# Kernel optimization log

Measured on AMD Instinct MI355X. Metric: run time of the kernel, lower is better.

Reference implementation:

```python
import jax, jax.numpy as jnp
import numpy as np

N, E, D, H, C, G = 80000, 1280000, 64, 64, 5, 512


def setup_inputs() -> dict:
    key = jax.random.key(0)
    ks = jax.random.split(key, 8)
    h = jax.random.normal(ks[0], (N, D), jnp.float32)
    src = jax.random.randint(ks[1], (E,), 0, N)
    dst = jax.random.randint(ks[2], (E,), 0, N)
    graph_ids = jnp.sort(jax.random.randint(ks[3], (N,), 0, G))
    # Glorot-ish init for weights
    W1 = jax.random.normal(ks[4], (D, H), jnp.float32) * (1.0 / np.sqrt(D))
    b1 = jnp.zeros((H,), jnp.float32)
    W2 = jax.random.normal(ks[5], (H, H), jnp.float32) * (1.0 / np.sqrt(H))
    b2 = jnp.zeros((H,), jnp.float32)
    Wc = jax.random.normal(ks[6], (H, C), jnp.float32) * (1.0 / np.sqrt(H))
    bc = jnp.zeros((C,), jnp.float32)
    return dict(h=h, src=src, dst=dst, graph_ids=graph_ids,
                W1=W1, b1=b1, W2=W2, b2=b2, Wc=Wc, bc=bc, num_graphs=G)


def reference(h, src, dst, graph_ids, W1, b1, W2, b2, Wc, bc, num_graphs):
    n = h.shape[0]
    ones_e = jnp.ones(src.shape[0], h.dtype)
    # DGL GraphConv norm='both': symmetric normalization, degrees clamped to >=1
    out_deg = jnp.clip(jax.ops.segment_sum(ones_e, src, num_segments=n), 1.0)
    in_deg = jnp.clip(jax.ops.segment_sum(ones_e, dst, num_segments=n), 1.0)
    norm_src = jax.lax.rsqrt(out_deg)  # [N]
    norm_dst = jax.lax.rsqrt(in_deg)   # [N]

    def graph_conv(x, W, b):
        x = x * norm_src[:, None]                                   # scale by D_out^{-1/2}
        agg = jax.ops.segment_sum(x[src], dst, num_segments=n)      # sparse A^T x (copy_u + sum)
        agg = agg * norm_dst[:, None]                               # scale by D_in^{-1/2}
        return agg @ W + b

    h1 = jax.nn.relu(graph_conv(h, W1, b1))
    h2 = jax.nn.relu(graph_conv(h1, W2, b2))

    # dgl.mean_nodes: per-graph mean pooling over nodes
    cnt = jnp.clip(jax.ops.segment_sum(jnp.ones(n, h.dtype), graph_ids,
                                       num_segments=num_graphs), 1.0)
    hg = jax.ops.segment_sum(h2, graph_ids, num_segments=num_graphs) / cnt[:, None]
    return hg @ Wc + bc  # [G, C] logits
```

## Files before the change

### kernel.cpp

```cpp
#include <hip/hip_runtime.h>
#include <hip/hip_bf16.h>


#define NBK 160
#define HB  256
#define CAP 9216

typedef __attribute__((ext_vector_type(8))) short bf16x8;
typedef __attribute__((ext_vector_type(4))) float f32x4;

__device__ __forceinline__ float bflo(unsigned u) { return __uint_as_float(u << 16); }
__device__ __forceinline__ float bfhi(unsigned u) { return __uint_as_float(u & 0xffff0000u); }
__device__ __forceinline__ float bf1(unsigned short u) { return __uint_as_float((unsigned)u << 16); }
__device__ __forceinline__ unsigned short f2bf(float f) {
    unsigned u = __float_as_uint(f);
    return (unsigned short)((u + 0x7fff + ((u >> 16) & 1)) >> 16);
}
__device__ __forceinline__ unsigned packbf(float lo, float hi) {
    return (unsigned)f2bf(lo) | ((unsigned)f2bf(hi) << 16);
}

__global__ __launch_bounds__(256) void pA_scatter(
    const int* __restrict__ src, const int* __restrict__ dst,
    int* __restrict__ curD, int* __restrict__ curS,
    int* __restrict__ pack, unsigned short* __restrict__ sloc,
    const int* __restrict__ gids, int* __restrict__ goffs,
    int E, int NB, int N, int G)
{
    if (blockIdx.x >= HB) {
        int i = (blockIdx.x - HB) * 256 + threadIdx.x;
        if (i >= N) return;
        int b = gids[i];
        if (i == 0) {
            for (int g = 0; g <= b; g++) goffs[g] = 0;
        } else {
            int a = gids[i - 1];
            for (int g = a + 1; g <= b; g++) goffs[g] = i;
        }
        if (i == N - 1) {
            for (int g = b + 1; g <= G; g++) goffs[g] = N;
        }
        return;
    }
    __shared__ int hd[NBK], hs[NBK];
    int t = threadIdx.x;
    for (int i = t; i < NB; i += 256) { hd[i] = 0; hs[i] = 0; }
    __syncthreads();
    int chunk = (E + HB - 1) / HB;
    int s0 = blockIdx.x * chunk, s1 = min(E, s0 + chunk);
    int q0 = s0 >> 2, q1 = s1 >> 2;
    const int4* s4 = (const int4*)src;
    const int4* d4 = (const int4*)dst;
    for (int q = q0 + t; q < q1; q += 256) {
        int4 d = d4[q];
        int4 s = s4[q];
        atomicAdd(&hd[d.x >> 9], 1); atomicAdd(&hd[d.y >> 9], 1);
        atomicAdd(&hd[d.z >> 9], 1); atomicAdd(&hd[d.w >> 9], 1);
        atomicAdd(&hs[s.x >> 9], 1); atomicAdd(&hs[s.y >> 9], 1);
        atomicAdd(&hs[s.z >> 9], 1); atomicAdd(&hs[s.w >> 9], 1);
    }
    for (int i = (q1 << 2) + t; i < s1; i += 256) {
        atomicAdd(&hd[dst[i] >> 9], 1);
        atomicAdd(&hs[src[i] >> 9], 1);
    }
    __syncthreads();
    for (int b = t; b < NB; b += 256) {
        int cd = hd[b], cs = hs[b];
        hd[b] = cd ? atomicAdd(&curD[b], cd) : 0;
        hs[b] = cs ? atomicAdd(&curS[b], cs) : 0;
    }
    __syncthreads();
    for (int q = q0 + t; q < q1; q += 256) {
        int4 d = d4[q];
        int4 s = s4[q];
        #pragma unroll
        for (int j = 0; j < 4; j++) {
            int ss = j == 0 ? s.x : j == 1 ? s.y : j == 2 ? s.z : s.w;
            int dd = j == 0 ? d.x : j == 1 ? d.y : j == 2 ? d.z : d.w;
            int bd = dd >> 9, bs = ss >> 9;
            int pd = atomicAdd(&hd[bd], 1);
            int ps = atomicAdd(&hs[bs], 1);
            if (pd < CAP) pack[(size_t)bd * CAP + pd] = ((dd & 511) << 17) | ss;
            if (ps < CAP) sloc[(size_t)bs * CAP + ps] = (unsigned short)(ss & 511);
        }
    }
    for (int i = (q1 << 2) + t; i < s1; i += 256) {
        int s = src[i], d = dst[i];
        int bd = d >> 9, bs = s >> 9;
        int pd = atomicAdd(&hd[bd], 1);
        int ps = atomicAdd(&hs[bs], 1);
        if (pd < CAP) pack[(size_t)bd * CAP + pd] = ((d & 511) << 17) | s;
        if (ps < CAP) sloc[(size_t)bs * CAP + ps] = (unsigned short)(s & 511);
    }
}

__global__ __launch_bounds__(256) void p5_build(
    const int* __restrict__ pack, const unsigned short* __restrict__ sloc,
    const int* __restrict__ curD, const int* __restrict__ curS,
    int* __restrict__ col, int* __restrict__ row_offs, int* __restrict__ deg,
    float* __restrict__ nsrc, float* __restrict__ ndst,
    const float* __restrict__ h, unsigned short* __restrict__ xs,
    int N, int NB)
{
    __shared__ int hist[512];
    __shared__ float nsl[512];
    __shared__ int wt[4];
    int t = threadIdx.x;
    bool dmode = blockIdx.x < NB;
    int b = dmode ? blockIdx.x : blockIdx.x - NB;
    int n0 = b << 9, n1 = min(N, n0 + 512);
    hist[t] = 0; hist[t + 256] = 0;
    __syncthreads();
    int e0 = b * CAP;
    int tot = min(dmode ? curD[b] : curS[b], CAP);
    int e1 = e0 + tot;
    if (!dmode) {
        for (int i = e0 + t; i < e1; i += 256)
            atomicAdd(&hist[sloc[i]], 1);
        __syncthreads();
        for (int n = n0 + t; n < n1; n += 256) {
            float s = rsqrtf((float)max(hist[n - n0], 1));
            nsrc[n] = s;
            nsl[n - n0] = s;
        }
        __syncthreads();
        int cnt = n1 - n0;
        const float2* h2p = (const float2*)h;
        ushort2* xp = (ushort2*)xs;
        for (int i = t; i < cnt * 32; i += 256) {
            int node = i >> 5;
            float s = nsl[node];
            float2 v = h2p[(size_t)(n0 + node) * 32 + (i & 31)];
            ushort2 o;
            o.x = f2bf(v.x * s);
            o.y = f2bf(v.y * s);
            xp[(size_t)(n0 + node) * 32 + (i & 31)] = o;
        }
        return;
    }
    for (int i = e0 + t; i < e1; i += 256)
        atomicAdd(&hist[pack[i] >> 17], 1);
    __syncthreads();
    int c0 = hist[2 * t], c1 = hist[2 * t + 1];
    int v = c0 + c1;
    int lane = t & 63, w = t >> 6;
    int x = v;
    #pragma unroll
    for (int off = 1; off < 64; off <<= 1) {
        int y = __shfl_up(x, off);
        if (lane >= off) x += y;
    }
    if (lane == 63) wt[w] = x;
    __syncthreads();
    int bw = 0;
    for (int i = 0; i < w; i++) bw += wt[i];
    int excl = x - v + bw;
    int n = n0 + 2 * t;
    if (n < n1) {
        row_offs[n] = e0 + excl;
        deg[n] = c0;
        ndst[n] = rsqrtf((float)max(c0, 1));
    }
    if (n + 1 < n1) {
        row_offs[n + 1] = e0 + excl + c0;
        deg[n + 1] = c1;
        ndst[n + 1] = rsqrtf((float)max(c1, 1));
    }
    hist[2 * t] = excl;
    hist[2 * t + 1] = excl + c0;
    __syncthreads();
    for (int i = e0 + t; i < e1; i += 256) {
        int wd = pack[i];
        int pos = atomicAdd(&hist[wd >> 17], 1);
        col[e0 + pos] = wd & 0x1FFFF;
    }
}

__global__ __launch_bounds__(256) void agg_kernel(
    const unsigned short* __restrict__ z, unsigned short* __restrict__ y,
    const int* __restrict__ col, const int* __restrict__ row_offs,
    const int* __restrict__ deg, int N)
{
    int lane = threadIdx.x & 63;
    int sub  = lane >> 3;
    int li   = lane & 7;
    const uint4* x4 = (const uint4*)z;

    int wid = (blockIdx.x * 256 + threadIdx.x) >> 6;
    int nw  = (gridDim.x * 256) >> 6;

    int ro = 0, cnt = 0, idx = 0;
    if (wid < N) {
        ro = row_offs[wid];
        cnt = deg[wid];
        if (lane < min(cnt, 64)) idx = col[ro + lane];
    }
    for (int node = wid; node < N; node += nw) {
        int nnode = node + nw;
        int nro = 0, ncnt = 0;
        if (nnode < N) { nro = row_offs[nnode]; ncnt = deg[nnode]; }

        float a0=0.f,a1=0.f,a2=0.f,a3=0.f,a4=0.f,a5=0.f,a6=0.f,a7=0.f;
        int cc = 0;
        int cidx = idx;
        while (cc < cnt) {
            int m = min(cnt - cc, 64);
            for (int i = 0; i < m; i += 32) {
                int e1 = i + sub, e2 = i + 8 + sub, e3 = i + 16 + sub, e4 = i + 24 + sub;
                int s1 = __shfl(cidx, min(e1, m - 1));
                int s2 = __shfl(cidx, min(e2, m - 1));
                int s3 = __shfl(cidx, min(e3, m - 1));
                int s4 = __shfl(cidx, min(e4, m - 1));
                uint4 v1 = make_uint4(0u,0u,0u,0u), v2 = v1, v3 = v1, v4 = v1;
                if (e1 < m) v1 = x4[(size_t)s1 * 8 + li];
                if (e2 < m) v2 = x4[(size_t)s2 * 8 + li];
                if (e3 < m) v3 = x4[(size_t)s3 * 8 + li];
                if (e4 < m) v4 = x4[(size_t)s4 * 8 + li];
                a0 += bflo(v1.x); a1 += bfhi(v1.x);
                a2 += bflo(v1.y); a3 += bfhi(v1.y);
                a4 += bflo(v1.z); a5 += bfhi(v1.z);
                a6 += bflo(v1.w); a7 += bfhi(v1.w);
                a0 += bflo(v2.x); a1 += bfhi(v2.x);
                a2 += bflo(v2.y); a3 += bfhi(v2.y);
                a4 += bflo(v2.z); a5 += bfhi(v2.z);
                a6 += bflo(v2.w); a7 += bfhi(v2.w);
                a0 += bflo(v3.x); a1 += bfhi(v3.x);
                a2 += bflo(v3.y); a3 += bfhi(v3.y);
                a4 += bflo(v3.z); a5 += bfhi(v3.z);
                a6 += bflo(v3.w); a7 += bfhi(v3.w);
                a0 += bflo(v4.x); a1 += bfhi(v4.x);
                a2 += bflo(v4.y); a3 += bfhi(v4.y);
                a4 += bflo(v4.z); a5 += bfhi(v4.z);
                a6 += bflo(v4.w); a7 += bfhi(v4.w);
            }
            cc += 64;
            if (cc < cnt) cidx = (lane < min(cnt - cc, 64)) ? col[ro + cc + lane] : 0;
        }
        idx = 0;
        if (nnode < N && lane < min(ncnt, 64)) idx = col[nro + lane];

        #pragma unroll
        for (int off = 8; off <= 32; off <<= 1) {
            a0 += __shfl_xor(a0, off); a1 += __shfl_xor(a1, off);
            a2 += __shfl_xor(a2, off); a3 += __shfl_xor(a3, off);
            a4 += __shfl_xor(a4, off); a5 += __shfl_xor(a5, off);
            a6 += __shfl_xor(a6, off); a7 += __shfl_xor(a7, off);
        }
        if (sub == 0) {
            uint4 o;
            o.x = packbf(a0, a1);
            o.y = packbf(a2, a3);
            o.z = packbf(a4, a5);
            o.w = packbf(a6, a7);
            ((uint4*)y)[(size_t)node * 8 + li] = o;
        }
        ro = nro; cnt = ncnt;
    }
}

template<int POOL>
__global__ __launch_bounds__(256) void gemm_kernel(
    const unsigned short* __restrict__ A, const float* __restrict__ W,
    const float* __restrict__ b, const float* __restrict__ ndst,
    const float* __restrict__ nsrc, unsigned short* __restrict__ Z,
    const int* __restrict__ gids, float* __restrict__ gacc, int M)
{
    int t = threadIdx.x, lane = t & 63, w = t >> 6;
    int col = lane & 15, quad = lane >> 4;
    bf16x8 bfrag[4][2];
    #pragma unroll
    for (int nt = 0; nt < 4; nt++)
        #pragma unroll
        for (int ks = 0; ks < 2; ks++)
            #pragma unroll
            for (int j = 0; j < 8; j++)
                bfrag[nt][ks][j] =
                    (short)f2bf(W[(ks * 32 + quad * 8 + j) * 64 + nt * 16 + col]);
    float bias[4];
    #pragma unroll
    for (int nt = 0; nt < 4; nt++) bias[nt] = b[nt * 16 + col];

    int mbase = blockIdx.x * 64 + w * 16;
    if (mbase >= M) return;
    int row = min(mbase + col, M - 1);
    const uint4* a4 = (const uint4*)A;
    union { uint4 u; bf16x8 v; } a0, a1;
    a0.u = a4[(size_t)row * 8 + quad];
    a1.u = a4[(size_t)row * 8 + 4 + quad];

    float nd[4], ns[4];
    int gg[4];
    #pragma unroll
    for (int r = 0; r < 4; r++) {
        int m = min(mbase + quad * 4 + r, M - 1);
        nd[r] = ndst[m];
        ns[r] = POOL ? 1.f : nsrc[m];
        gg[r] = POOL ? gids[m] : 0;
    }
    bool uni = false;
    int g0 = 0;
    if (POOL) {
        g0 = gids[min(mbase, M - 1)];
        uni = (g0 == gids[min(mbase + 15, M - 1)]) && (mbase + 15 < M);
    }

    #pragma unroll
    for (int nt = 0; nt < 4; nt++) {
        f32x4 acc = {0.f, 0.f, 0.f, 0.f};
        acc = __builtin_amdgcn_mfma_f32_16x16x32_bf16(a0.v, bfrag[nt][0], acc, 0, 0, 0);
        acc = __builtin_amdgcn_mfma_f32_16x16x32_bf16(a1.v, bfrag[nt][1], acc, 0, 0, 0);
        if (POOL) {
            float vv[4];
            #pragma unroll
            for (int r = 0; r < 4; r++) {
                int m = mbase + quad * 4 + r;
                vv[r] = (m < M) ? fmaxf(nd[r] * acc[r] + bias[nt], 0.f) : 0.f;
            }
            if (uni) {
                float s = (vv[0] + vv[1]) + (vv[2] + vv[3]);
                s += __shfl_xor(s, 16);
                s += __shfl_xor(s, 32);
                if (quad == 0)
                    atomicAdd(&gacc[(size_t)g0 * 64 + nt * 16 + col], s);
            } else {
                #pragma unroll
                for (int r = 0; r < 4; r++) {
                    int m = mbase + quad * 4 + r;
                    if (m < M)
                        atomicAdd(&gacc[(size_t)gg[r] * 64 + nt * 16 + col], vv[r]);
                }
            }
        } else {
            #pragma unroll
            for (int r = 0; r < 4; r++) {
                int m = mbase + quad * 4 + r;
                if (m < M) {
                    float v = fmaxf(nd[r] * acc[r] + bias[nt], 0.f);
                    Z[(size_t)m * 64 + nt * 16 + col] = f2bf(v * ns[r]);
                }
            }
        }
    }
}

__global__ __launch_bounds__(64) void cls_kernel(
    const float* __restrict__ gacc, const int* __restrict__ goffs,
    const float* __restrict__ Wc, const float* __restrict__ bc,
    float* __restrict__ out, int G)
{
    int g = blockIdx.x;
    int lane = threadIdx.x;
    float cnt = (float)max(goffs[g + 1] - goffs[g], 1);
    float mean = gacc[(size_t)g * 64 + lane] / cnt;
    #pragma unroll
    for (int c = 0; c < 5; c++) {
        float p = mean * Wc[lane * 5 + c];
        #pragma unroll
        for (int off = 32; off; off >>= 1) p += __shfl_down(p, off);
        if (lane == 0) out[g * 5 + c] = p + bc[c];
    }
}

extern "C" void kernel_launch(void* const* d_in, const int* in_sizes, int n_in,
                              void* d_out, int out_size, void* d_ws, size_t ws_size,
                              hipStream_t stream)
{
    const float* h    = (const float*)d_in[0];
    const int*   src  = (const int*)d_in[1];
    const int*   dst  = (const int*)d_in[2];
    const int*   gids = (const int*)d_in[3];
    const float* W1   = (const float*)d_in[4];
    const float* b1   = (const float*)d_in[5];
    const float* W2   = (const float*)d_in[6];
    const float* b2   = (const float*)d_in[7];
    const float* Wc   = (const float*)d_in[8];
    const float* bc   = (const float*)d_in[9];
    float* out = (float*)d_out;

    const int N = in_sizes[0] / 64;
    const int E = in_sizes[1];
    const int G = out_size / 5;
    const int NB = (N + 511) >> 9;
    const int NBB = (N + 255) / 256;

    auto align = [](size_t x) { return (x + 255) & ~(size_t)255; };
    char* p = (char*)d_ws;
    int* curD    = (int*)p;
    int* curS    = curD + NBK;
    float* gacc  = (float*)(p + (size_t)2 * NBK * 4);
    size_t zbytes = (size_t)2 * NBK * 4 + (size_t)G * 64 * 4;
    p += align(zbytes);
    int* row_offs= (int*)p;            p += align((size_t)N * 4);
    int* deg     = (int*)p;            p += align((size_t)N * 4);
    float* nsrc  = (float*)p;          p += align((size_t)N * 4);
    float* ndst  = (float*)p;          p += align((size_t)N * 4);
    int* goffs   = (int*)p;            p += align((size_t)(G + 1) * 4);
    int* pack    = (int*)p;            p += align((size_t)NBK * CAP * 4);
    unsigned short* sloc = (unsigned short*)p; p += align((size_t)NBK * CAP * 2);
    int* cols    = (int*)p;            p += align((size_t)NBK * CAP * 4);
    unsigned short* xs  = (unsigned short*)p; p += align((size_t)N * 64 * 2);
    unsigned short* s1  = (unsigned short*)p; p += align((size_t)N * 64 * 2);
    unsigned short* h1s = (unsigned short*)p; p += align((size_t)N * 64 * 2);
    unsigned short* s2  = s1;

    hipMemsetAsync(curD, 0, zbytes, stream);

    pA_scatter<<<HB + NBB, 256, 0, stream>>>(src, dst, curD, curS, pack, sloc,
                                             gids, goffs, E, NB, N, G);
    p5_build<<<2 * NB, 256, 0, stream>>>(pack, sloc, curD, curS, cols,
                                         row_offs, deg, nsrc, ndst, h, xs, N, NB);

    agg_kernel<<<4096, 256, 0, stream>>>(xs, s1, cols, row_offs, deg, N);
    gemm_kernel<0><<<(N + 63) / 64, 256, 0, stream>>>(s1, W1, b1, ndst, nsrc,
                                                      h1s, nullptr, nullptr, N);
    agg_kernel<<<4096, 256, 0, stream>>>(h1s, s2, cols, row_offs, deg, N);
    gemm_kernel<1><<<(N + 63) / 64, 256, 0, stream>>>(s2, W2, b2, ndst, nullptr,
                                                      nullptr, gids, gacc, N);
    cls_kernel<<<G, 64, 0, stream>>>(gacc, goffs, Wc, bc, out, G);
}
```

Baseline: 216.5 us.

## Prefetch next node's first gathers in aggregation; fuse classifier into pooling GEMM

The aggregation kernel now issues the first 32 neighbor-row gathers for the next node before reducing and storing the current node. This hides some gather latency across loop iterations at the cost of extra live registers. Separately, the classifier kernel is removed. The last block of the pooling GEMM, chosen with a global ticket counter and threadfence, computes the per-graph means and logits, saving one launch but serializing that tail work onto a single block.

```diff
diff --git a/kernel.cpp b/kernel.cpp
--- a/kernel.cpp
+++ b/kernel.cpp
@@ -176,6 +176,12 @@
     }
 }
 
+#define UNPACK8S(v)                                       \
+    a0 += bflo(v.x); a1 += bfhi(v.x);                     \
+    a2 += bflo(v.y); a3 += bfhi(v.y);                     \
+    a4 += bflo(v.z); a5 += bfhi(v.z);                     \
+    a6 += bflo(v.w); a7 += bfhi(v.w);
+
 __global__ __launch_bounds__(256) void agg_kernel(
     const unsigned short* __restrict__ z, unsigned short* __restrict__ y,
     const int* __restrict__ col, const int* __restrict__ row_offs,
@@ -185,15 +191,27 @@
     int sub  = lane >> 3;
     int li   = lane & 7;
     const uint4* x4 = (const uint4*)z;
+    const uint4 z4 = make_uint4(0u, 0u, 0u, 0u);
 
     int wid = (blockIdx.x * 256 + threadIdx.x) >> 6;
     int nw  = (gridDim.x * 256) >> 6;
 
     int ro = 0, cnt = 0, idx = 0;
+    uint4 pv1 = z4, pv2 = z4, pv3 = z4, pv4 = z4;
     if (wid < N) {
         ro = row_offs[wid];
         cnt = deg[wid];
         if (lane < min(cnt, 64)) idx = col[ro + lane];
+        int m = min(cnt, 64), mm = min(m, 32);
+        int e1 = sub, e2 = 8 + sub, e3 = 16 + sub, e4 = 24 + sub;
+        int s1 = __shfl(idx, min(e1, m - 1) & 63);
+        int s2 = __shfl(idx, min(e2, m - 1) & 63);
+        int s3 = __shfl(idx, min(e3, m - 1) & 63);
+        int s4 = __shfl(idx, min(e4, m - 1) & 63);
+        if (e1 < mm) pv1 = x4[(size_t)s1 * 8 + li];
+        if (e2 < mm) pv2 = x4[(size_t)s2 * 8 + li];
+        if (e3 < mm) pv3 = x4[(size_t)s3 * 8 + li];
+        if (e4 < mm) pv4 = x4[(size_t)s4 * 8 + li];
     }
     for (int node = wid; node < N; node += nw) {
         int nnode = node + nw;
@@ -201,43 +219,58 @@
         if (nnode < N) { nro = row_offs[nnode]; ncnt = deg[nnode]; }
 
         float a0=0.f,a1=0.f,a2=0.f,a3=0.f,a4=0.f,a5=0.f,a6=0.f,a7=0.f;
-        int cc = 0;
-        int cidx = idx;
-        while (cc < cnt) {
-            int m = min(cnt - cc, 64);
-            for (int i = 0; i < m; i += 32) {
-                int e1 = i + sub, e2 = i + 8 + sub, e3 = i + 16 + sub, e4 = i + 24 + sub;
-                int s1 = __shfl(cidx, min(e1, m - 1));
-                int s2 = __shfl(cidx, min(e2, m - 1));
-                int s3 = __shfl(cidx, min(e3, m - 1));
-                int s4 = __shfl(cidx, min(e4, m - 1));
-                uint4 v1 = make_uint4(0u,0u,0u,0u), v2 = v1, v3 = v1, v4 = v1;
+        {
+            int m = min(cnt, 64);
+            UNPACK8S(pv1); UNPACK8S(pv2); UNPACK8S(pv3); UNPACK8S(pv4);
+            if (m > 32) {
+                int e1 = 32 + sub, e2 = 40 + sub, e3 = 48 + sub, e4 = 56 + sub;
+                int s1 = __shfl(idx, min(e1, m - 1));
+                int s2 = __shfl(idx, min(e2, m - 1));
+                int s3 = __shfl(idx, min(e3, m - 1));
+                int s4 = __shfl(idx, min(e4, m - 1));
+                uint4 v1 = z4, v2 = z4, v3 = z4, v4 = z4;
                 if (e1 < m) v1 = x4[(size_t)s1 * 8 + li];
                 if (e2 < m) v2 = x4[(size_t)s2 * 8 + li];
                 if (e3 < m) v3 = x4[(size_t)s3 * 8 + li];
                 if (e4 < m) v4 = x4[(size_t)s4 * 8 + li];
-                a0 += bflo(v1.x); a1 += bfhi(v1.x);
-                a2 += bflo(v1.y); a3 += bfhi(v1.y);
-                a4 += bflo(v1.z); a5 += bfhi(v1.z);
-                a6 += bflo(v1.w); a7 += bfhi(v1.w);
-                a0 += bflo(v2.x); a1 += bfhi(v2.x);
-                a2 += bflo(v2.y); a3 += bfhi(v2.y);
-                a4 += bflo(v2.z); a5 += bfhi(v2.z);
-                a6 += bflo(v2.w); a7 += bfhi(v2.w);
-                a0 += bflo(v3.x); a1 += bfhi(v3.x);
-                a2 += bflo(v3.y); a3 += bfhi(v3.y);
-                a4 += bflo(v3.z); a5 += bfhi(v3.z);
-                a6 += bflo(v3.w); a7 += bfhi(v3.w);
-                a0 += bflo(v4.x); a1 += bfhi(v4.x);
-                a2 += bflo(v4.y); a3 += bfhi(v4.y);
-                a4 += bflo(v4.z); a5 += bfhi(v4.z);
-                a6 += bflo(v4.w); a7 += bfhi(v4.w);
+                UNPACK8S(v1); UNPACK8S(v2); UNPACK8S(v3); UNPACK8S(v4);
             }
-            cc += 64;
-            if (cc < cnt) cidx = (lane < min(cnt - cc, 64)) ? col[ro + cc + lane] : 0;
-        }
+            int cc = 64;
+            while (cc < cnt) {
+                int m2 = min(cnt - cc, 64);
+                int cidx = (lane < m2) ? col[ro + cc + lane] : 0;
+                for (int i = 0; i < m2; i += 32) {
+                    int e1 = i + sub, e2 = i + 8 + sub, e3 = i + 16 + sub, e4 = i + 24 + sub;
+                    int s1 = __shfl(cidx, min(e1, m2 - 1));
+                    int s2 = __shfl(cidx, min(e2, m2 - 1));
+                    int s3 = __shfl(cidx, min(e3, m2 - 1));
+                    int s4 = __shfl(cidx, min(e4, m2 - 1));
+                    uint4 v1 = z4, v2 = z4, v3 = z4, v4 = z4;
+                    if (e1 < m2) v1 = x4[(size_t)s1 * 8 + li];
+                    if (e2 < m2) v2 = x4[(size_t)s2 * 8 + li];
+                    if (e3 < m2) v3 = x4[(size_t)s3 * 8 + li];
+                    if (e4 < m2) v4 = x4[(size_t)s4 * 8 + li];
+                    UNPACK8S(v1); UNPACK8S(v2); UNPACK8S(v3); UNPACK8S(v4);
+                }
+                cc += 64;
+            }
+        }
+
         idx = 0;
         if (nnode < N && lane < min(ncnt, 64)) idx = col[nro + lane];
+        pv1 = z4; pv2 = z4; pv3 = z4; pv4 = z4;
+        {
+            int m = min(ncnt, 64), mm = min(m, 32);
+            int e1 = sub, e2 = 8 + sub, e3 = 16 + sub, e4 = 24 + sub;
+            int s1 = __shfl(idx, min(e1, m - 1) & 63);
+            int s2 = __shfl(idx, min(e2, m - 1) & 63);
+            int s3 = __shfl(idx, min(e3, m - 1) & 63);
+            int s4 = __shfl(idx, min(e4, m - 1) & 63);
+            if (e1 < mm) pv1 = x4[(size_t)s1 * 8 + li];
+            if (e2 < mm) pv2 = x4[(size_t)s2 * 8 + li];
+            if (e3 < mm) pv3 = x4[(size_t)s3 * 8 + li];
+            if (e4 < mm) pv4 = x4[(size_t)s4 * 8 + li];
+        }
 
         #pragma unroll
         for (int off = 8; off <= 32; off <<= 1) {
@@ -263,8 +296,12 @@
     const unsigned short* __restrict__ A, const float* __restrict__ W,
     const float* __restrict__ b, const float* __restrict__ ndst,
     const float* __restrict__ nsrc, unsigned short* __restrict__ Z,
-    const int* __restrict__ gids, float* __restrict__ gacc, int M)
+    const int* __restrict__ gids, float* __restrict__ gacc,
+    int* __restrict__ ticket, const int* __restrict__ goffs,
+    const float* __restrict__ Wc, const float* __restrict__ bc,
+    float* __restrict__ out, int M, int G)
 {
+    __shared__ int lastf;
     int t = threadIdx.x, lane = t & 63, w = t >> 6;
     int col = lane & 15, quad = lane >> 4;
     bf16x8 bfrag[4][2];
@@ -281,83 +318,89 @@
     for (int nt = 0; nt < 4; nt++) bias[nt] = b[nt * 16 + col];
 
     int mbase = blockIdx.x * 64 + w * 16;
-    if (mbase >= M) return;
-    int row = min(mbase + col, M - 1);
-    const uint4* a4 = (const uint4*)A;
-    union { uint4 u; bf16x8 v; } a0, a1;
-    a0.u = a4[(size_t)row * 8 + quad];
-    a1.u = a4[(size_t)row * 8 + 4 + quad];
-
-    float nd[4], ns[4];
-    int gg[4];
-    #pragma unroll
-    for (int r = 0; r < 4; r++) {
-        int m = min(mbase + quad * 4 + r, M - 1);
-        nd[r] = ndst[m];
-        ns[r] = POOL ? 1.f : nsrc[m];
-        gg[r] = POOL ? gids[m] : 0;
-    }
-    bool uni = false;
-    int g0 = 0;
-    if (POOL) {
-        g0 = gids[min(mbase, M - 1)];
-        uni = (g0 == gids[min(mbase + 15, M - 1)]) && (mbase + 15 < M);
-    }
-
-    #pragma unroll
-    for (int nt = 0; nt < 4; nt++) {
-        f32x4 acc = {0.f, 0.f, 0.f, 0.f};
-        acc = __builtin_amdgcn_mfma_f32_16x16x32_bf16(a0.v, bfrag[nt][0], acc, 0, 0, 0);
-        acc = __builtin_amdgcn_mfma_f32_16x16x32_bf16(a1.v, bfrag[nt][1], acc, 0, 0, 0);
+    if (mbase < M) {
+        int row = min(mbase + col, M - 1);
+        const uint4* a4 = (const uint4*)A;
+        union { uint4 u; bf16x8 v; } a0, a1;
+        a0.u = a4[(size_t)row * 8 + quad];
+        a1.u = a4[(size_t)row * 8 + 4 + quad];
+
+        float nd[4], ns[4];
+        int gg[4];
+        #pragma unroll
+        for (int r = 0; r < 4; r++) {
+            int m = min(mbase + quad * 4 + r, M - 1);
+            nd[r] = ndst[m];
+            ns[r] = POOL ? 1.f : nsrc[m];
+            gg[r] = POOL ? gids[m] : 0;
+        }
+        bool uni = false;
+        int g0 = 0;
         if (POOL) {
-            float vv[4];
-            #pragma unroll
-            for (int r = 0; r < 4; r++) {
-                int m = mbase + quad * 4 + r;
-                vv[r] = (m < M) ? fmaxf(nd[r] * acc[r] + bias[nt], 0.f) : 0.f;
-            }
-            if (uni) {
-                float s = (vv[0] + vv[1]) + (vv[2] + vv[3]);
-                s += __shfl_xor(s, 16);
-                s += __shfl_xor(s, 32);
-                if (quad == 0)
-                    atomicAdd(&gacc[(size_t)g0 * 64 + nt * 16 + col], s);
+            g0 = gids[min(mbase, M - 1)];
+            uni = (g0 == gids[min(mbase + 15, M - 1)]) && (mbase + 15 < M);
+        }
+
+        #pragma unroll
+        for (int nt = 0; nt < 4; nt++) {
+            f32x4 acc = {0.f, 0.f, 0.f, 0.f};
+            acc = __builtin_amdgcn_mfma_f32_16x16x32_bf16(a0.v, bfrag[nt][0], acc, 0, 0, 0);
+            acc = __builtin_amdgcn_mfma_f32_16x16x32_bf16(a1.v, bfrag[nt][1], acc, 0, 0, 0);
+            if (POOL) {
+                float vv[4];
+                #pragma unroll
+                for (int r = 0; r < 4; r++) {
+                    int m = mbase + quad * 4 + r;
+                    vv[r] = (m < M) ? fmaxf(nd[r] * acc[r] + bias[nt], 0.f) : 0.f;
+                }
+                if (uni) {
+                    float s = (vv[0] + vv[1]) + (vv[2] + vv[3]);
+                    s += __shfl_xor(s, 16);
+                    s += __shfl_xor(s, 32);
+                    if (quad == 0)
+                        atomicAdd(&gacc[(size_t)g0 * 64 + nt * 16 + col], s);
+                } else {
+                    #pragma unroll
+                    for (int r = 0; r < 4; r++) {
+                        int m = mbase + quad * 4 + r;
+                        if (m < M)
+                            atomicAdd(&gacc[(size_t)gg[r] * 64 + nt * 16 + col], vv[r]);
+                    }
+                }
             } else {
                 #pragma unroll
                 for (int r = 0; r < 4; r++) {
                     int m = mbase + quad * 4 + r;
-                    if (m < M)
-                        atomicAdd(&gacc[(size_t)gg[r] * 64 + nt * 16 + col], vv[r]);
+                    if (m < M) {
+                        float v = fmaxf(nd[r] * acc[r] + bias[nt], 0.f);
+                        Z[(size_t)m * 64 + nt * 16 + col] = f2bf(v * ns[r]);
+                    }
                 }
             }
-        } else {
-            #pragma unroll
-            for (int r = 0; r < 4; r++) {
-                int m = mbase + quad * 4 + r;
-                if (m < M) {
-                    float v = fmaxf(nd[r] * acc[r] + bias[nt], 0.f);
-                    Z[(size_t)m * 64 + nt * 16 + col] = f2bf(v * ns[r]);
+        }
+    }
+
+    if (POOL) {
+        __threadfence();
+        __syncthreads();
+        if (t == 0) lastf = (atomicAdd(ticket, 1) == (int)gridDim.x - 1);
+        __syncthreads();
+        if (lastf) {
+            for (int g = w; g < G; g += 4) {
+                float cnt = (float)max(goffs[g + 1] - goffs[g], 1);
+                float v = __hip_atomic_load(&gacc[(size_t)g * 64 + lane],
+                                            __ATOMIC_RELAXED,
+                                            __HIP_MEMORY_SCOPE_AGENT);
+                float mean = v / cnt;
+                #pragma unroll
+                for (int c = 0; c < 5; c++) {
+                    float p = mean * Wc[lane * 5 + c];
+                    #pragma unroll
+                    for (int off = 32; off; off >>= 1) p += __shfl_down(p, off);
+                    if (lane == 0) out[g * 5 + c] = p + bc[c];
                 }
             }
         }
-    }
-}
-
-__global__ __launch_bounds__(64) void cls_kernel(
-    const float* __restrict__ gacc, const int* __restrict__ goffs,
-    const float* __restrict__ Wc, const float* __restrict__ bc,
-    float* __restrict__ out, int G)
-{
-    int g = blockIdx.x;
-    int lane = threadIdx.x;
-    float cnt = (float)max(goffs[g + 1] - goffs[g], 1);
-    float mean = gacc[(size_t)g * 64 + lane] / cnt;
-    #pragma unroll
-    for (int c = 0; c < 5; c++) {
-        float p = mean * Wc[lane * 5 + c];
-        #pragma unroll
-        for (int off = 32; off; off >>= 1) p += __shfl_down(p, off);
-        if (lane == 0) out[g * 5 + c] = p + bc[c];
     }
 }
 
@@ -387,8 +430,10 @@
     char* p = (char*)d_ws;
     int* curD    = (int*)p;
     int* curS    = curD + NBK;
-    float* gacc  = (float*)(p + (size_t)2 * NBK * 4);
-    size_t zbytes = (size_t)2 * NBK * 4 + (size_t)G * 64 * 4;
+    int* ticket  = curD + 2 * NBK;
+    size_t cur_bytes = align((size_t)(2 * NBK + 1) * 4);
+    float* gacc  = (float*)(p + cur_bytes);
+    size_t zbytes = cur_bytes + (size_t)G * 64 * 4;
     p += align(zbytes);
     int* row_offs= (int*)p;            p += align((size_t)N * 4);
     int* deg     = (int*)p;            p += align((size_t)N * 4);
@@ -411,10 +456,11 @@
                                          row_offs, deg, nsrc, ndst, h, xs, N, NB);
 
     agg_kernel<<<4096, 256, 0, stream>>>(xs, s1, cols, row_offs, deg, N);
-    gemm_kernel<0><<<(N + 63) / 64, 256, 0, stream>>>(s1, W1, b1, ndst, nsrc,
-                                                      h1s, nullptr, nullptr, N);
+    gemm_kernel<0><<<(N + 63) / 64, 256, 0, stream>>>(
+        s1, W1, b1, ndst, nsrc, h1s, nullptr, nullptr,
+        nullptr, nullptr, nullptr, nullptr, nullptr, N, G);
     agg_kernel<<<4096, 256, 0, stream>>>(h1s, s2, cols, row_offs, deg, N);
-    gemm_kernel<1><<<(N + 63) / 64, 256, 0, stream>>>(s2, W2, b2, ndst, nullptr,
-                                                      nullptr, gids, gacc, N);
-    cls_kernel<<<G, 64, 0, stream>>>(gacc, goffs, Wc, bc, out, G);
-}
+    gemm_kernel<1><<<(N + 63) / 64, 256, 0, stream>>>(
+        s2, W2, b2, ndst, nullptr, nullptr, gids, gacc,
+        ticket, goffs, Wc, bc, out, N, G);
+}
```

Measured after the change: 448.5 us. +107.1%, slower.

## Switch aggregation to lane-per-feature gathers with scalar readlane indices

Applied to the files above, without the earlier changes.

Restructures the gather-sum kernel so each of the 64 lanes owns one feature column and all lanes read the same neighbor row, broadcasting neighbor indices with readlane instead of shuffles. This removes the cross-lane shuffle-xor reduction and the uint4 repacking. In exchange each lane issues 2-byte loads, so there are many more load instructions per edge, although each row access is still one coalesced 128-byte read. Only 8 rows are in flight per iteration instead of 32.

```diff
diff --git a/kernel.cpp b/kernel.cpp
--- a/kernel.cpp
+++ b/kernel.cpp
@@ -15,9 +15,6 @@
 __device__ __forceinline__ unsigned short f2bf(float f) {
     unsigned u = __float_as_uint(f);
     return (unsigned short)((u + 0x7fff + ((u >> 16) & 1)) >> 16);
-}
-__device__ __forceinline__ unsigned packbf(float lo, float hi) {
-    return (unsigned)f2bf(lo) | ((unsigned)f2bf(hi) << 16);
 }
 
 __global__ __launch_bounds__(256) void pA_scatter(
@@ -182,78 +179,62 @@
     const int* __restrict__ deg, int N)
 {
     int lane = threadIdx.x & 63;
-    int sub  = lane >> 3;
-    int li   = lane & 7;
-    const uint4* x4 = (const uint4*)z;
 
     int wid = (blockIdx.x * 256 + threadIdx.x) >> 6;
     int nw  = (gridDim.x * 256) >> 6;
 
-    int ro = 0, cnt = 0, idx = 0;
+    int ro = 0, cnt = 0, cidx = 0;
     if (wid < N) {
         ro = row_offs[wid];
         cnt = deg[wid];
-        if (lane < min(cnt, 64)) idx = col[ro + lane];
+        if (lane < min(cnt, 64)) cidx = col[ro + lane];
     }
     for (int node = wid; node < N; node += nw) {
         int nnode = node + nw;
         int nro = 0, ncnt = 0;
         if (nnode < N) { nro = row_offs[nnode]; ncnt = deg[nnode]; }
 
-        float a0=0.f,a1=0.f,a2=0.f,a3=0.f,a4=0.f,a5=0.f,a6=0.f,a7=0.f;
+        float acc = 0.f;
         int cc = 0;
-        int cidx = idx;
+        int cur = cidx;
         while (cc < cnt) {
             int m = min(cnt - cc, 64);
-            for (int i = 0; i < m; i += 32) {
-                int e1 = i + sub, e2 = i + 8 + sub, e3 = i + 16 + sub, e4 = i + 24 + sub;
-                int s1 = __shfl(cidx, min(e1, m - 1));
-                int s2 = __shfl(cidx, min(e2, m - 1));
-                int s3 = __shfl(cidx, min(e3, m - 1));
-                int s4 = __shfl(cidx, min(e4, m - 1));
-                uint4 v1 = make_uint4(0u,0u,0u,0u), v2 = v1, v3 = v1, v4 = v1;
-                if (e1 < m) v1 = x4[(size_t)s1 * 8 + li];
-                if (e2 < m) v2 = x4[(size_t)s2 * 8 + li];
-                if (e3 < m) v3 = x4[(size_t)s3 * 8 + li];
-                if (e4 < m) v4 = x4[(size_t)s4 * 8 + li];
-                a0 += bflo(v1.x); a1 += bfhi(v1.x);
-                a2 += bflo(v1.y); a3 += bfhi(v1.y);
-                a4 += bflo(v1.z); a5 += bfhi(v1.z);
-                a6 += bflo(v1.w); a7 += bfhi(v1.w);
-                a0 += bflo(v2.x); a1 += bfhi(v2.x);
-                a2 += bflo(v2.y); a3 += bfhi(v2.y);
-                a4 += bflo(v2.z); a5 += bfhi(v2.z);
-                a6 += bflo(v2.w); a7 += bfhi(v2.w);
-                a0 += bflo(v3.x); a1 += bfhi(v3.x);
-                a2 += bflo(v3.y); a3 += bfhi(v3.y);
-                a4 += bflo(v3.z); a5 += bfhi(v3.z);
-                a6 += bflo(v3.w); a7 += bfhi(v3.w);
-                a0 += bflo(v4.x); a1 += bfhi(v4.x);
-                a2 += bflo(v4.y); a3 += bfhi(v4.y);
-                a4 += bflo(v4.z); a5 += bfhi(v4.z);
-                a6 += bflo(v4.w); a7 += bfhi(v4.w);
+            int e = 0;
+            for (; e + 8 <= m; e += 8) {
+                int s0 = __builtin_amdgcn_readlane(cur, e);
+                int s1 = __builtin_amdgcn_readlane(cur, e + 1);
+                int s2 = __builtin_amdgcn_readlane(cur, e + 2);
+                int s3 = __builtin_amdgcn_readlane(cur, e + 3);
+                int s4 = __builtin_amdgcn_readlane(cur, e + 4);
+                int s5 = __builtin_amdgcn_readlane(cur, e + 5);
+                int s6 = __builtin_amdgcn_readlane(cur, e + 6);
+                int s7 = __builtin_amdgcn_readlane(cur, e + 7);
+                unsigned short u0 = z[(size_t)s0 * 64 + lane];
+                unsigned short u1 = z[(size_t)s1 * 64 + lane];
+                unsigned short u2 = z[(size_t)s2 * 64 + lane];
+                unsigned short u3 = z[(size_t)s3 * 64 + lane];
+                unsigned short u4 = z[(size_t)s4 * 64 + lane];
+                unsigned short u5 = z[(size_t)s5 * 64 + lane];
+                unsigned short u6 = z[(size_t)s6 * 64 + lane];
+                unsigned short u7 = z[(size_t)s7 * 64 + lane];
+                float t0 = bf1(u0) + bf1(u1);
+                float t1 = bf1(u2) + bf1(u3);
+                float t2 = bf1(u4) + bf1(u5);
+                float t3 = bf1(u6) + bf1(u7);
+                acc += (t0 + t1) + (t2 + t3);
+            }
+            for (; e < m; e++) {
+                int s = __builtin_amdgcn_readlane(cur, e);
+                acc += bf1(z[(size_t)s * 64 + lane]);
             }
             cc += 64;
-            if (cc < cnt) cidx = (lane < min(cnt - cc, 64)) ? col[ro + cc + lane] : 0;
-        }
-        idx = 0;
-        if (nnode < N && lane < min(ncnt, 64)) idx = col[nro + lane];
-
-        #pragma unroll
-        for (int off = 8; off <= 32; off <<= 1) {
-            a0 += __shfl_xor(a0, off); a1 += __shfl_xor(a1, off);
-            a2 += __shfl_xor(a2, off); a3 += __shfl_xor(a3, off);
-            a4 += __shfl_xor(a4, off); a5 += __shfl_xor(a5, off);
-            a6 += __shfl_xor(a6, off); a7 += __shfl_xor(a7, off);
-        }
-        if (sub == 0) {
-            uint4 o;
-            o.x = packbf(a0, a1);
-            o.y = packbf(a2, a3);
-            o.z = packbf(a4, a5);
-            o.w = packbf(a6, a7);
-            ((uint4*)y)[(size_t)node * 8 + li] = o;
-        }
+            if (cc < cnt) cur = (lane < min(cnt - cc, 64)) ? col[ro + cc + lane] : 0;
+        }
+
+        cidx = 0;
+        if (nnode < N && lane < min(ncnt, 64)) cidx = col[nro + lane];
+
+        y[(size_t)node * 64 + lane] = f2bf(acc);
         ro = nro; cnt = ncnt;
     }
 }
```

New measurement: 225.4 us. 1.04x slower.
